# Optimization experiments

Hardware: AMD Instinct MI355X
Metric: run time of the kernel (lower is better)

The kernel has to match this reference:

```python
import jax, jax.numpy as jnp
import numpy as np

H = 256          # encoder hidden per direction
D = 2 * H        # decoder hidden / bidirectional feature dim
IN = 2
OUT = 2
B = 64
T = 256
STEPS = 24       # hard-coded decoder loop length in the source


def gru_cell(x, h, Wih, Whh, bih, bhh):
    # PyTorch GRU cell: gate order (r, z, n)
    gi = x @ Wih.T + bih
    gh = h @ Whh.T + bhh
    ir, iz, inn = jnp.split(gi, 3, axis=-1)
    hr, hz, hn = jnp.split(gh, 3, axis=-1)
    r = jax.nn.sigmoid(ir + hr)
    z = jax.nn.sigmoid(iz + hz)
    n = jnp.tanh(inn + r * hn)
    return (1.0 - z) * n + z * h


def run_dir(xs, Wih, Whh, bih, bhh, reverse):
    # xs: (T, B, F) time-major; returns outputs (T, B, H) and last hidden (B, H)
    h0 = jnp.zeros((xs.shape[1], Whh.shape[-1]), xs.dtype)
    def step(h, xt):
        h2 = gru_cell(xt, h, Wih, Whh, bih, bhh)
        return h2, h2
    h_last, ys = jax.lax.scan(step, h0, xs, reverse=reverse)
    return ys, h_last


def setup_inputs():
    keys = jax.random.split(jax.random.key(0), 24)
    k = iter(keys)
    def rn(shape, s):
        return jax.random.normal(next(k), shape, jnp.float32) * s
    se = 1.0 / np.sqrt(H)
    sd = 1.0 / np.sqrt(D)
    return {
        "x": rn((B, T, IN), 1.0),
        "enc_Wih0": rn((2, 3 * H, IN), se),
        "enc_Whh0": rn((2, 3 * H, H), se),
        "enc_bih0": rn((2, 3 * H), se),
        "enc_bhh0": rn((2, 3 * H), se),
        "enc_Wih": rn((2, 2, 3 * H, D), se),
        "enc_Whh": rn((2, 2, 3 * H, H), se),
        "enc_bih": rn((2, 2, 3 * H), se),
        "enc_bhh": rn((2, 2, 3 * H), se),
        "dec_Wih": rn((3, 3 * D, D), sd),
        "dec_Whh": rn((3, 3 * D, D), sd),
        "dec_bih": rn((3, 3 * D), sd),
        "dec_bhh": rn((3, 3 * D), sd),
        "fc_con_W": rn((D, 2 * D), sd),
        "fc_con_b": rn((D,), sd),
        "attn_W": rn((D, 2 * D), sd),
        "attn_b": rn((D,), sd),
        "v": jax.random.uniform(next(k), (D,), jnp.float32),  # torch.rand init
        "fc_W": rn((OUT, D), sd),
        "fc_b": rn((OUT,), sd),
    }


def reference(x, enc_Wih0, enc_Whh0, enc_bih0, enc_bhh0,
              enc_Wih, enc_Whh, enc_bih, enc_bhh,
              dec_Wih, dec_Whh, dec_bih, dec_bhh,
              fc_con_W, fc_con_b, attn_W, attn_b, v, fc_W, fc_b):
    # ---- bidirectional 3-layer GRU encoder ----
    seq = x.transpose(1, 0, 2)  # (T, B, IN) time-major
    hf_list, hb_list = [], []
    for l in range(3):
        if l == 0:
            Wf, Uf, bf, cf = enc_Wih0[0], enc_Whh0[0], enc_bih0[0], enc_bhh0[0]
            Wb, Ub, bb, cb = enc_Wih0[1], enc_Whh0[1], enc_bih0[1], enc_bhh0[1]
        else:
            Wf, Uf, bf, cf = enc_Wih[l-1, 0], enc_Whh[l-1, 0], enc_bih[l-1, 0], enc_bhh[l-1, 0]
            Wb, Ub, bb, cb = enc_Wih[l-1, 1], enc_Whh[l-1, 1], enc_bih[l-1, 1], enc_bhh[l-1, 1]
        yf, hf = run_dir(seq, Wf, Uf, bf, cf, False)
        yb, hb = run_dir(seq, Wb, Ub, bb, cb, True)
        seq = jnp.concatenate([yf, yb], axis=-1)
        hf_list.append(hf)
        hb_list.append(hb)
    enc_out = seq.transpose(1, 0, 2)  # (B, T, D)
    # hidden_decoder = cat(forward, backward) per layer -> (3, B, D)
    hidden = jnp.stack([jnp.concatenate([f, b], axis=-1)
                        for f, b in zip(hf_list, hb_list)])
    dec_in = enc_out[:, -1, :]  # (B, D)

    # additive attention: energy = tanh(W [h; enc_out] + b); precompute enc part
    attn_Wh = attn_W[:, :D]
    attn_We = attn_W[:, D:]
    enc_proj = jnp.einsum('bte,de->btd', enc_out, attn_We)  # (B, T, D)

    def dec_step(carry, _):
        d_in, hid = carry
        hq = hid[-1] @ attn_Wh.T                               # (B, D)
        energy = jnp.tanh(hq[:, None, :] + enc_proj + attn_b)  # (B, T, D)
        scores = jnp.einsum('btd,d->bt', energy, v)
        aw = jax.nn.softmax(scores, axis=1)                    # (B, T)
        ctx = jnp.einsum('bt,btd->bd', aw, enc_out)            # (B, D)
        inp = jnp.concatenate([d_in, ctx], axis=-1) @ fc_con_W.T + fc_con_b
        new_h = []
        for l in range(3):  # 3-layer unidirectional decoder GRU, single step
            hl = gru_cell(inp, hid[l], dec_Wih[l], dec_Whh[l], dec_bih[l], dec_bhh[l])
            new_h.append(hl)
            inp = hl
        out_step = inp @ fc_W.T + fc_b
        return (inp, jnp.stack(new_h)), out_step

    _, outs = jax.lax.scan(dec_step, (dec_in, hidden), None, length=STEPS)
    return outs.transpose(1, 0, 2)  # (B, 24, OUT)
```

## Files before the change

kernel.cpp:

```cpp
#include <hip/hip_runtime.h>

typedef unsigned short u16;
typedef unsigned int u32;
typedef _Float16 f16;
typedef f16   f16x2 __attribute__((ext_vector_type(2)));
typedef f16   f16x4 __attribute__((ext_vector_type(4)));
typedef f16   f16x8 __attribute__((ext_vector_type(8)));
typedef float f32x4 __attribute__((ext_vector_type(4)));

#define MFMA16(a,b,c) __builtin_amdgcn_mfma_f32_16x16x32_f16((a),(b),(c),0,0,0)

__device__ __forceinline__ float sigm_(float x){ return 1.f/(1.f + __expf(-x)); }
__device__ __forceinline__ float tanh_(float x){ return 1.f - 2.f/(1.f + __expf(2.f*x)); }
__device__ __forceinline__ float clampf(float x, float c){
  if (!(x > -c)) x = -c;
  if (x > c) x = c;
  return x;
}
__device__ __forceinline__ f16x8 cvt8f(const float* p){
  const float4 a = *(const float4*)p;
  const float4 b = *(const float4*)(p+4);
  f16x8 r;
  r[0]=(f16)a.x; r[1]=(f16)a.y; r[2]=(f16)a.z; r[3]=(f16)a.w;
  r[4]=(f16)b.x; r[5]=(f16)b.y; r[6]=(f16)b.z; r[7]=(f16)b.w;
  return r;
}

__device__ __forceinline__ void gbar_(u32* c, u32 nb){
  __syncthreads();
  __threadfence();
  if (threadIdx.x == 0) {
    __hip_atomic_fetch_add(c, 1u, __ATOMIC_RELAXED, __HIP_MEMORY_SCOPE_AGENT);
    while (__hip_atomic_load(c, __ATOMIC_RELAXED, __HIP_MEMORY_SCOPE_AGENT) < nb) {}
  }
  __syncthreads();
  __threadfence();
}

__global__ void k_diag(float* out, int mib){
  const int i = blockIdx.x*256 + threadIdx.x;
  if (i < 3072) out[i] = 1000.f * (float)mib;
}

__global__ void k_prep_dec(const float* dWhh, const float* attnW, const float* fccon,
                           const float* dWih, f16* R3)
{
  long idx = (long)blockIdx.x*256 + threadIdx.x;
  const float* src; int rs, colOff = 0, NKS; long dst, loc;
  if (idx < 294912L) {
    loc = idx; const int m = (int)(loc / 98304); loc %= 98304;
    src = dWhh + (long)m*786432; rs = 512; NKS = 16; dst = (long)m*786432;
  } else if (idx < 327680L) {
    loc = idx - 294912L; src = attnW; colOff = 512; rs = 1024; NKS = 16; dst = 2359296L;
  } else if (idx < 393216L) {
    loc = idx - 327680L; src = fccon; rs = 1024; NKS = 32; dst = 2621440L;
  } else if (idx < 688128L) {
    loc = idx - 393216L; const int m = (int)(loc / 98304); loc %= 98304;
    src = dWih + (long)m*786432; rs = 512; NKS = 16; dst = 3440640L + (long)m*786432;
  } else if (idx < 720896L) {
    loc = idx - 688128L; src = attnW; colOff = 0; rs = 1024; NKS = 16; dst = 5799936L;
  } else return;
  const int lane = (int)(loc & 63);
  const long frag = loc >> 6;
  const int ks = (int)(frag % NKS);
  const long nt = frag / NKS;
  const int n  = (int)(nt*16 + (lane & 15));
  const int k0 = ks*32 + ((lane >> 4) << 3);
  const float* sp = src + (long)n*rs + colOff + k0;
  f16* dp = R3 + dst + loc*8;
  #pragma unroll
  for (int j = 0; j < 8; ++j) dp[j] = (f16)sp[j];
}

__global__ void k_gi0s(const float* __restrict__ x, const float* __restrict__ W,
                       const float* __restrict__ bi, f16* __restrict__ gi,
                       int seg, int BH, int lbh, int b0)
{
  const long idx = (long)blockIdx.x*256 + threadIdx.x;
  const int v = (int)(idx % 24);
  long rest = idx / 24;
  const int tid = (int)(rest & 511); rest >>= 9;
  const int bq = (int)(rest & ((1 << (lbh-4)) - 1)); rest >>= (lbh-4);
  const int s = (int)(rest & 63);
  const int d = (int)(rest >> 6);
  const int r = v / 6, rem = v % 6, i = rem / 3, g = rem % 3;
  const int w = tid >> 6, q = (tid >> 4) & 3, lo = tid & 15;
  const int n = g*256 + (2*w + i)*16 + lo;
  const int b = bq*16 + q*4 + r;
  const int t = d ? (255 - (seg*64 + s)) : (seg*64 + s);
  const float x0 = x[(((b0+b)<<8) + t)*2];
  const float x1 = x[(((b0+b)<<8) + t)*2 + 1];
  const long wi = ((long)d*768 + n)*2;
  gi[idx] = (f16)clampf(x0*W[wi] + x1*W[wi+1] + bi[d*768 + n], 32.f);
}

#define GIE(G, vv) ((float)((vv) < 8 ? (G)[0][(vv)&7] : ((vv) < 16 ? (G)[1][(vv)-8] : (G)[2][(vv)-16])))

__global__ __launch_bounds__(512, 1) void k_enc_seg(
    const f16* __restrict__ gi, const float* __restrict__ Wraw,
    const float* __restrict__ bhh, f16* __restrict__ seq, int ostr,
    f16* __restrict__ fin, float* __restrict__ hcar, int seg, int BH)
{
  const int tid = threadIdx.x;
  const int w = tid >> 6, lane = tid & 63;
  const int lo16 = lane & 15, quad = lane >> 4;
  const int nbq = BH >> 4;
  const int dir = blockIdx.x / nbq, bq = blockIdx.x % nbq;

  __shared__ f16 h16[4][16][264];

  const float* mat = Wraw + (long)dir*196608;
  f16x8 wr[6][8];
  #pragma unroll
  for (int p = 0; p < 3; ++p)
    #pragma unroll
    for (int i = 0; i < 2; ++i) {
      const int n = (p*16 + 2*w + i)*16 + lo16;
      #pragma unroll
      for (int ks = 0; ks < 8; ++ks)
        wr[p*2+i][ks] = cvt8f(mat + (long)n*256 + ks*32 + quad*8);
    }
  float bh_[3][2];
  #pragma unroll
  for (int p = 0; p < 3; ++p)
    #pragma unroll
    for (int i = 0; i < 2; ++i)
      bh_[p][i] = bhh[dir*768 + p*256 + (2*w+i)*16 + lo16];

  float hreg[2][4];
  if (seg == 0) {
    #pragma unroll
    for (int i = 0; i < 2; ++i)
      #pragma unroll
      for (int r = 0; r < 4; ++r) {
        hreg[i][r] = 0.f;
        h16[0][quad*4 + r][(2*w+i)*16 + lo16] = (f16)0.f;
      }
  } else {
    #pragma unroll
    for (int i = 0; i < 2; ++i) {
      const int c = (2*w+i)*16 + lo16;
      #pragma unroll
      for (int r = 0; r < 4; ++r) {
        const float v = hcar[((dir*BH) + bq*16 + quad*4 + r)*256 + c];
        hreg[i][r] = v;
        h16[0][quad*4 + r][c] = (f16)v;
      }
    }
  }

  const long gstep = (long)nbq*512*24;
  const f16* gbase = gi + (((long)dir*64*nbq + bq)*512 + tid)*24;
  f16x8 g0[3], g1[3];
  { const f16x8* gp = (const f16x8*)gbase; g0[0]=gp[0]; g0[1]=gp[1]; g0[2]=gp[2]; }

  const int frow = tid >> 5;
  const int fcol = (tid & 31) * 8;

  for (int s = 0; s < 64; ++s) {
    __syncthreads();
    if (s >= 2) {
      const int so = s - 2;
      const int t2 = dir ? (255 - (seg*64 + so)) : (seg*64 + so);
      const f16x8 hv = *(const f16x8*)&h16[(so+1)&3][frow][fcol];
      *(f16x8*)&seq[((long)t2*ostr + bq*16 + frow)*512 + dir*256 + fcol] = hv;
    }
    f32x4 acc[6];
    #pragma unroll
    for (int q = 0; q < 6; ++q) acc[q] = (f32x4){0.f,0.f,0.f,0.f};
    #pragma unroll
    for (int ks = 0; ks < 8; ++ks) {
      const f16x8 a = *(const f16x8*)&h16[s&3][lo16][ks*32 + quad*8];
      #pragma unroll
      for (int q = 0; q < 6; ++q)
        acc[q] = MFMA16(a, wr[q][ks], acc[q]);
    }
    if (s < 63) {
      const f16x8* gp = (const f16x8*)(gbase + (long)(s+1)*gstep);
      g1[0]=gp[0]; g1[1]=gp[1]; g1[2]=gp[2];
    }
    #pragma unroll
    for (int i = 0; i < 2; ++i) {
      const int c = (2*w+i)*16 + lo16;
      #pragma unroll
      for (int r = 0; r < 4; ++r) {
        const int row = quad*4 + r;
        const int v = r*6 + i*3;
        const float gir = GIE(g0, v);
        const float giz = GIE(g0, v+1);
        const float gin = GIE(g0, v+2);
        const float rv = sigm_(gir + acc[i][r]   + bh_[0][i]);
        const float zv = sigm_(giz + acc[2+i][r] + bh_[1][i]);
        const float nv = tanh_(gin + rv*(acc[4+i][r] + bh_[2][i]));
        float hn = (1.f - zv)*nv + zv*hreg[i][r];
        hn = clampf(hn, 2.f);
        hreg[i][r] = hn;
        h16[(s+1)&3][row][c] = (f16)hn;
        if (seg == 3 && s == 63) fin[(bq*16 + row)*512 + dir*256 + c] = (f16)hn;
      }
    }
    g0[0]=g1[0]; g0[1]=g1[1]; g0[2]=g1[2];
  }
  __syncthreads();
  #pragma unroll
  for (int so = 62; so < 64; ++so) {
    const int t2 = dir ? (255 - (seg*64 + so)) : (seg*64 + so);
    const f16x8 hv = *(const f16x8*)&h16[(so+1)&3][frow][fcol];
    *(f16x8*)&seq[((long)t2*ostr + bq*16 + frow)*512 + dir*256 + fcol] = hv;
  }
  #pragma unroll
  for (int i = 0; i < 2; ++i) {
    const int c = (2*w+i)*16 + lo16;
    #pragma unroll
    for (int r = 0; r < 4; ++r)
      hcar[((dir*BH) + bq*16 + quad*4 + r)*256 + c] = hreg[i][r];
  }
}

__global__ void k_gemm_gi(const f16* __restrict__ A,
                          const float* __restrict__ Braw, long bzs,
                          const float* __restrict__ bias,
                          f16* __restrict__ gi,
                          int tb0, int tb1, int tdirsgn, int abstr, float cv)
{
  const int tid = threadIdx.x, w = tid>>6, lane = tid&63;
  const int lo16 = lane&15, quad = lane>>4;
  const int s_ = blockIdx.x;
  const int y  = blockIdx.y;
  const int z  = blockIdx.z;
  const int tbase = z ? tb1 : tb0;
  const int tdir  = z ? -tdirsgn : tdirsgn;
  const int mrow = s_*64 + w*16 + lo16;
  const long arow = (long)(tbase + tdir*(mrow >> 6))*abstr + (mrow & 63);
  const f16* Ap = A + arow*512 + quad*8;
  const float* Bp = Braw + (long)z*bzs;
  f32x4 acc[12];
  #pragma unroll
  for (int i=0;i<12;++i) acc[i]=(f32x4){0.f,0.f,0.f,0.f};
  for (int ks = 0; ks < 16; ++ks) {
    const f16x8 a = *(const f16x8*)(Ap + ks*32);
    #pragma unroll
    for (int g = 0; g < 3; ++g)
      #pragma unroll
      for (int jj = 0; jj < 4; ++jj) {
        const int n = g*256 + y*64 + jj*16 + lo16;
        const f16x8 b = cvt8f(Bp + (long)n*512 + ks*32 + quad*8);
        acc[g*4+jj] = MFMA16(a, b, acc[g*4+jj]);
      }
  }
  f16* base = gi + (((long)z*64 + s_)*4 + w)*12288L;
  #pragma unroll
  for (int l = 0; l < 2; ++l) {
    f16x8 rec8[3];
    #pragma unroll
    for (int r = 0; r < 4; ++r)
      #pragma unroll
      for (int jl = 0; jl < 2; ++jl)
        #pragma unroll
        for (int g = 0; g < 3; ++g) {
          const int nt = g*4 + l*2 + jl;
          const int n = g*256 + y*64 + (l*2+jl)*16 + lo16;
          const int slot = r*6 + jl*3 + g;
          rec8[slot>>3][slot&7] = (f16)clampf(acc[nt][r] + bias[z*768 + n], cv);
        }
    f16* dp = base + ((long)(y*2 + l)*64 + quad*16 + lo16)*24L;
    *(f16x8*)(dp)      = rec8[0];
    *(f16x8*)(dp + 8)  = rec8[1];
    *(f16x8*)(dp + 16) = rec8[2];
  }
}

__global__ void k_gemm(const f16* __restrict__ A, int K,
                       const f16* __restrict__ Bsw, const float* __restrict__ Braw,
                       long bzs, int ldb, int koff,
                       const float* __restrict__ bias, int biaszs,
                       void* __restrict__ Cv, long czs, int ldc, int mode,
                       int tb0, int tb1, int tdirsgn, int lbh, int abstr, float cv)
{
  const int tid = threadIdx.x, w = tid>>6, lane = tid&63;
  const int lo16 = lane&15, quad = lane>>4;
  const int m0 = blockIdx.x*64 + w*16;
  const int n0 = blockIdx.y*128;
  const int z  = blockIdx.z;
  const int tbase = z ? tb1 : tb0;
  const int tdir  = z ? -tdirsgn : tdirsgn;
  const int NKS = K >> 5;
  const int mrow = m0 + lo16;
  const long arow = (long)(tbase + tdir*(mrow >> lbh))*abstr + (mrow & ((1<<lbh)-1));
  const f16* Ap = A + arow*K + quad*8;
  f32x4 acc[8];
  #pragma unroll
  for (int i=0;i<8;++i) acc[i]=(f32x4){0.f,0.f,0.f,0.f};
  if (Bsw) {
    const f16* Bp = Bsw + (long)z*bzs;
    for (int ks = 0; ks < NKS; ++ks) {
      const f16x8 a = *(const f16x8*)(Ap + ks*32);
      #pragma unroll
      for (int nt = 0; nt < 8; ++nt) {
        const f16x8 b = *(const f16x8*)(Bp + (((long)((n0>>4)+nt)*NKS + ks) << 9) + lane*8);
        acc[nt] = MFMA16(a, b, acc[nt]);
      }
    }
  } else {
    const float* Bp = Braw + (long)z*bzs;
    for (int ks = 0; ks < NKS; ++ks) {
      const f16x8 a = *(const f16x8*)(Ap + ks*32);
      #pragma unroll
      for (int nt = 0; nt < 8; ++nt) {
        const f16x8 b = cvt8f(Bp + (long)(n0 + nt*16 + lo16)*ldb + koff + ks*32 + quad*8);
        acc[nt] = MFMA16(a, b, acc[nt]);
      }
    }
  }
  #pragma unroll
  for (int nt = 0; nt < 8; ++nt) {
    const int n = n0 + nt*16 + lo16;
    const float bv = bias ? bias[z*biaszs + n] : 0.f;
    #pragma unroll
    for (int r = 0; r < 4; ++r) {
      const int m = m0 + quad*4 + r;
      const float val = clampf(acc[nt][r] + bv, cv);
      if (mode == 2) {
        const int s_ = m >> lbh, b_ = m & ((1<<lbh)-1);
        const int bq_ = b_ >> 4, q_ = (b_ >> 2) & 3, r_ = b_ & 3;
        const int g_ = n >> 8, j_ = (n >> 4) & 15, lo_ = n & 15;
        const long idx = ((((long)z*64 + s_)*(1<<(lbh-4)) + bq_)*512
                          + ((j_>>1)*64 + q_*16 + lo_))*24 + r_*6 + (j_&1)*3 + g_;
        ((f16*)Cv)[idx] = (f16)val;
      } else if (mode == 1)
        ((f16*)Cv)[(long)z*czs + (long)m*ldc + n] = (f16)val;
      else
        ((float*)Cv)[(long)z*czs + (long)m*ldc + n] = val;
    }
  }
}

__global__ void k_score(const f16* __restrict__ seq, const f16* __restrict__ We,
                        const float* __restrict__ hq, const float* __restrict__ ab,
                        const float* __restrict__ vp, float* __restrict__ S)
{
  const int t = blockIdx.x, tid = threadIdx.x;
  const int w = tid>>6, lane = tid&63, lo16 = lane&15, quad = lane>>4;
  __shared__ float svab[1024];
  for (int i = tid; i < 512; i += 256) { svab[i] = vp[i]; svab[512+i] = ab[i]; }
  __syncthreads();
  f32x4 acc[32];
  #pragma unroll
  for (int i=0;i<32;++i) acc[i]=(f32x4){0.f,0.f,0.f,0.f};
  const f16* Ap = seq + ((long)t*64 + w*16 + lo16)*512 + quad*8;
  for (int ks = 0; ks < 16; ++ks) {
    const f16x8 a = *(const f16x8*)(Ap + ks*32);
    #pragma unroll
    for (int nt = 0; nt < 32; ++nt) {
      const f16x8 b = *(const f16x8*)(We + (((long)nt*16 + ks) << 9) + lane*8);
      acc[nt] = MFMA16(a, b, acc[nt]);
    }
  }
  #pragma unroll
  for (int r = 0; r < 4; ++r) {
    const int b = w*16 + quad*4 + r;
    float sc = 0.f;
    #pragma unroll
    for (int nt = 0; nt < 32; ++nt) {
      const int n = nt*16 + lo16;
      sc += svab[n] * tanh_(acc[nt][r] + hq[(b<<9) + n] + svab[512+n]);
    }
    sc += __shfl_xor(sc, 1, 64); sc += __shfl_xor(sc, 2, 64);
    sc += __shfl_xor(sc, 4, 64); sc += __shfl_xor(sc, 8, 64);
    if (lo16 == 0) S[(b<<8) + t] = clampf(sc, 256.f);
  }
}

__global__ void k_attnctx(const float* __restrict__ S, const f16* __restrict__ enc,
                          f16* __restrict__ cat)
{
  const int b = blockIdx.x, tid = threadIdx.x;
  __shared__ float ssc[256], srd[256];
  const float sc = clampf(S[(b<<8) + tid], 256.f);
  srd[tid] = sc; __syncthreads();
  for (int off = 128; off > 0; off >>= 1) { if (tid < off) srd[tid] = fmaxf(srd[tid], srd[tid+off]); __syncthreads(); }
  const float mx = srd[0]; __syncthreads();
  const float e = __expf(sc - mx);
  srd[tid] = e; __syncthreads();
  for (int off = 128; off > 0; off >>= 1) { if (tid < off) srd[tid] += srd[tid+off]; __syncthreads(); }
  const float inv = 1.f / srd[0]; __syncthreads();
  ssc[tid] = e * inv; __syncthreads();
  float c0 = 0.f, c1 = 0.f;
  for (int tt = 0; tt < 256; ++tt) {
    const float awt = ssc[tt];
    const f16* ep = enc + (((long)tt*64 + b) << 9);
    c0 += awt * (float)ep[tid];
    c1 += awt * (float)ep[256 + tid];
  }
  cat[(b<<10) + 512 + tid] = (f16)clampf(c0, 4.f);
  cat[(b<<10) + 768 + tid] = (f16)clampf(c1, 4.f);
}

__global__ void k_dec_init(const f16* __restrict__ fin, const f16* __restrict__ seq,
                           f16* __restrict__ hb16, float* __restrict__ hf32,
                           f16* __restrict__ cat, u32* __restrict__ cnt)
{
  const int idx = blockIdx.x*256 + threadIdx.x;
  if (idx < 64) cnt[idx] = 0;
  const int d = idx & 511, b = (idx >> 9) & 63, l = idx >> 15;
  if (l < 3) {
    const float v = clampf((float)fin[((long)l<<15) + (b<<9) + d], 2.f);
    hb16[(long)l*65536 + (b<<9) + d] = (f16)v;
    hf32[(long)l*32768 + (b<<9) + d] = v;
  } else {
    cat[(b<<10) + d] = seq[((long)255*64 + b)*512 + d];
  }
}

__global__ __launch_bounds__(512, 1) void k_attn(
    const f16* __restrict__ seq, const f16* __restrict__ ep,
    const float* __restrict__ hf2, const f16* __restrict__ cat,
    const f16* __restrict__ whsw, const f16* __restrict__ fcsw,
    const float* __restrict__ fcconB, const float* __restrict__ vp,
    f16* __restrict__ inp, const float* __restrict__ fcW,
    const float* __restrict__ fcb, float* __restrict__ out, int step)
{
  const int b = blockIdx.x;
  const int tid = threadIdx.x, w = tid >> 6, lane = tid & 63;
  const int quad = lane >> 4;
  __shared__ float hsm[512];
  __shared__ float cats[1024];
  __shared__ float hqs[512];
  __shared__ float aw[256];
  __shared__ float red[8*512];
  hsm[tid]  = hf2[(b<<9) + tid];
  cats[tid] = (float)cat[(b<<10) + tid];
  __syncthreads();
  if (w < 2 && step > 0) {
    float p = 0.f;
    #pragma unroll
    for (int j = 0; j < 8; ++j) p += fcW[(w<<9) + lane*8 + j] * hsm[lane*8 + j];
    p += __shfl_xor(p,1,64); p += __shfl_xor(p,2,64); p += __shfl_xor(p,4,64);
    p += __shfl_xor(p,8,64); p += __shfl_xor(p,16,64); p += __shfl_xor(p,32,64);
    if (lane == 0) out[(b*24 + step-1)*2 + w] = clampf(p + fcb[w], 128.f);
  }
  #pragma unroll
  for (int i = 0; i < 4; ++i) {
    const int nt = w*4 + i;
    float p = 0.f;
    for (int ks = 0; ks < 16; ++ks) {
      const f16x8 wv = *(const f16x8*)(whsw + (((long)nt*16 + ks)<<9) + lane*8);
      const float4 ha = *(const float4*)&hsm[ks*32 + quad*8];
      const float4 hb = *(const float4*)&hsm[ks*32 + quad*8 + 4];
      p += (float)wv[0]*ha.x + (float)wv[1]*ha.y + (float)wv[2]*ha.z + (float)wv[3]*ha.w
         + (float)wv[4]*hb.x + (float)wv[5]*hb.y + (float)wv[6]*hb.z + (float)wv[7]*hb.w;
    }
    p += __shfl_xor(p,16,64); p += __shfl_xor(p,32,64);
    if (lane < 16) hqs[nt*16 + lane] = p;
  }
  __syncthreads();
  float hq8[8], v8[8];
  #pragma unroll
  for (int j = 0; j < 8; ++j) { hq8[j] = hqs[lane*8+j]; v8[j] = vp[lane*8+j]; }
  #pragma unroll 2
  for (int i = 0; i < 32; ++i) {
    const int t = w*32 + i;
    const f16x8 e = *(const f16x8*)(ep + (((long)t*64 + b)<<9) + lane*8);
    float s = 0.f;
    #pragma unroll
    for (int j = 0; j < 8; ++j) s += v8[j]*tanh_((float)e[j] + hq8[j]);
    s += __shfl_xor(s,1,64); s += __shfl_xor(s,2,64); s += __shfl_xor(s,4,64);
    s += __shfl_xor(s,8,64); s += __shfl_xor(s,16,64); s += __shfl_xor(s,32,64);
    if (lane == 0) aw[t] = clampf(s, 256.f);
  }
  __syncthreads();
  if (tid < 64) {
    float s0=aw[tid], s1=aw[tid+64], s2=aw[tid+128], s3=aw[tid+192];
    float mx = fmaxf(fmaxf(s0,s1), fmaxf(s2,s3));
    mx = fmaxf(mx, __shfl_xor(mx,1,64)); mx = fmaxf(mx, __shfl_xor(mx,2,64));
    mx = fmaxf(mx, __shfl_xor(mx,4,64)); mx = fmaxf(mx, __shfl_xor(mx,8,64));
    mx = fmaxf(mx, __shfl_xor(mx,16,64)); mx = fmaxf(mx, __shfl_xor(mx,32,64));
    const float e0=__expf(s0-mx), e1=__expf(s1-mx), e2=__expf(s2-mx), e3=__expf(s3-mx);
    float sm = e0+e1+e2+e3;
    sm += __shfl_xor(sm,1,64); sm += __shfl_xor(sm,2,64); sm += __shfl_xor(sm,4,64);
    sm += __shfl_xor(sm,8,64); sm += __shfl_xor(sm,16,64); sm += __shfl_xor(sm,32,64);
    const float inv = 1.f/sm;
    aw[tid]=e0*inv; aw[tid+64]=e1*inv; aw[tid+128]=e2*inv; aw[tid+192]=e3*inv;
  }
  __syncthreads();
  float c8[8];
  #pragma unroll
  for (int j = 0; j < 8; ++j) c8[j] = 0.f;
  #pragma unroll 2
  for (int i = 0; i < 32; ++i) {
    const int t = w*32 + i;
    const f16x8 e = *(const f16x8*)(seq + (((long)t*64 + b)<<9) + lane*8);
    const float awt = aw[t];
    #pragma unroll
    for (int j = 0; j < 8; ++j) c8[j] += awt*(float)e[j];
  }
  #pragma unroll
  for (int j = 0; j < 8; ++j) red[(w<<9) + lane*8 + j] = c8[j];
  __syncthreads();
  {
    float s = 0.f;
    #pragma unroll
    for (int ww = 0; ww < 8; ++ww) s += red[(ww<<9) + tid];
    cats[512 + tid] = clampf(s, 4.f);
  }
  __syncthreads();
  #pragma unroll
  for (int i = 0; i < 4; ++i) {
    const int nt = w*4 + i;
    float p = 0.f;
    for (int ks = 0; ks < 32; ++ks) {
      const f16x8 wv = *(const f16x8*)(fcsw + (((long)nt*32 + ks)<<9) + lane*8);
      const float4 ca = *(const float4*)&cats[ks*32 + quad*8];
      const float4 cb = *(const float4*)&cats[ks*32 + quad*8 + 4];
      p += (float)wv[0]*ca.x + (float)wv[1]*ca.y + (float)wv[2]*ca.z + (float)wv[3]*ca.w
         + (float)wv[4]*cb.x + (float)wv[5]*cb.y + (float)wv[6]*cb.z + (float)wv[7]*cb.w;
    }
    p += __shfl_xor(p,16,64); p += __shfl_xor(p,32,64);
    if (lane < 16) inp[(b<<9) + nt*16 + lane] = (f16)clampf(p + fcconB[nt*16+lane], 64.f);
  }
}

__global__ void k_cell3(const f16* __restrict__ inp0, const f16* __restrict__ WihSw,
                        const f16* __restrict__ WhhSw, const float* __restrict__ bihA,
                        const float* __restrict__ bhhA, float* __restrict__ hfA,
                        f16* __restrict__ hb, f16* __restrict__ cat, int p, u32* cnt)
{
  const int tid = threadIdx.x, w = tid>>6, lane = tid&63;
  const int lo16 = lane&15, quad = lane>>4;
  const int Wt  = ((int)blockIdx.x & 7)*4 + w;
  const int mi0 = ((int)blockIdx.x >> 3)*2;
  for (int l = 0; l < 3; ++l) {
    const f16* inp = (l == 0) ? inp0 : (hb + (long)(2*(l-1) + (1-p))*32768);
    const f16* WihL = WihSw + (long)l*786432;
    const f16* WhhL = WhhSw + (long)l*786432;
    const float* bih = bihA + l*1536;
    const float* bhh = bhhA + l*1536;
    float* hf32 = hfA + (long)l*32768;
    const f16* hin = hb + (long)(2*l + p)*32768;
    f16* hout = hb + (long)(2*l + (1-p))*32768;
    f16* catp = (l == 2) ? cat : (f16*)nullptr;

    f32x4 arz[4], an_[4];
    #pragma unroll
    for (int i=0;i<4;++i){ arz[i]=(f32x4){0.f,0.f,0.f,0.f}; an_[i]=(f32x4){0.f,0.f,0.f,0.f}; }
    #pragma unroll 2
    for (int kk = 0; kk < 16; ++kk) {
      const f16x8 b0 = *(const f16x8*)(WihL + (((long)Wt*16 + kk)<<9)      + lane*8);
      const f16x8 b1 = *(const f16x8*)(WihL + (((long)(32+Wt)*16 + kk)<<9) + lane*8);
      const f16x8 b2 = *(const f16x8*)(WihL + (((long)(64+Wt)*16 + kk)<<9) + lane*8);
      #pragma unroll
      for (int m = 0; m < 2; ++m) {
        const f16x8 a = *(const f16x8*)&inp[(((mi0+m)*16 + lo16)<<9) + kk*32 + quad*8];
        arz[m]   = MFMA16(a, b0, arz[m]);
        arz[2+m] = MFMA16(a, b1, arz[2+m]);
        an_[m]   = MFMA16(a, b2, an_[m]);
      }
    }
    #pragma unroll 2
    for (int kk = 0; kk < 16; ++kk) {
      const f16x8 b0 = *(const f16x8*)(WhhL + (((long)Wt*16 + kk)<<9)      + lane*8);
      const f16x8 b1 = *(const f16x8*)(WhhL + (((long)(32+Wt)*16 + kk)<<9) + lane*8);
      const f16x8 b2 = *(const f16x8*)(WhhL + (((long)(64+Wt)*16 + kk)<<9) + lane*8);
      #pragma unroll
      for (int m = 0; m < 2; ++m) {
        const f16x8 a = *(const f16x8*)&hin[(((mi0+m)*16 + lo16)<<9) + kk*32 + quad*8];
        arz[m]   = MFMA16(a, b0, arz[m]);
        arz[2+m] = MFMA16(a, b1, arz[2+m]);
        an_[2+m] = MFMA16(a, b2, an_[2+m]);
      }
    }
    const int c = Wt*16 + lo16;
    const float brz0 = bih[c]     + bhh[c];
    const float brz1 = bih[512+c] + bhh[512+c];
    const float bin_ = bih[1024+c];
    const float bhn_ = bhh[1024+c];
    #pragma unroll
    for (int m = 0; m < 2; ++m)
      #pragma unroll
      for (int r = 0; r < 4; ++r) {
        const int row = (mi0+m)*16 + quad*4 + r;
        const float rv = sigm_(clampf(arz[m][r],64.f)   + brz0);
        const float zv = sigm_(clampf(arz[2+m][r],64.f) + brz1);
        const float nv = tanh_(clampf(an_[m][r],64.f) + bin_ + rv*(clampf(an_[2+m][r],64.f) + bhn_));
        const float ho = hf32[(row<<9) + c];
        float hn2 = (1.f - zv)*nv + zv*ho;
        hn2 = clampf(hn2, 2.f);
        hf32[(row<<9) + c] = hn2;
        hout[(row<<9) + c] = (f16)hn2;
        if (catp) catp[(row<<10) + c] = (f16)hn2;
      }
    if (l < 2) gbar_(cnt + l, 16);
  }
}

__global__ void k_cell_raw(const f16* __restrict__ inp, const float* __restrict__ WihRaw,
                           const f16* __restrict__ WhhSw, const float* __restrict__ bih,
                           const float* __restrict__ bhh, float* __restrict__ hf32,
                           const f16* __restrict__ hin, f16* __restrict__ hout,
                           f16* __restrict__ cat)
{
  const int tid = threadIdx.x, w = tid>>6, lane = tid&63;
  const int lo16 = lane&15, quad = lane>>4;
  const int Wt = blockIdx.x*4 + w;
  f32x4 arz[8], an_[8];
  #pragma unroll
  for (int i=0;i<8;++i){ arz[i]=(f32x4){0.f,0.f,0.f,0.f}; an_[i]=(f32x4){0.f,0.f,0.f,0.f}; }
  const int nr = Wt*16 + lo16;
  const float* Rr = WihRaw + (long)nr*512        + quad*8;
  const float* Rz = WihRaw + (long)(512+nr)*512  + quad*8;
  const float* Rn = WihRaw + (long)(1024+nr)*512 + quad*8;
  #pragma unroll 2
  for (int kk = 0; kk < 16; ++kk) {
    const f16x8 b0 = cvt8f(Rr + kk*32);
    const f16x8 b1 = cvt8f(Rz + kk*32);
    const f16x8 b2 = cvt8f(Rn + kk*32);
    #pragma unroll
    for (int mi = 0; mi < 4; ++mi) {
      const f16x8 a = *(const f16x8*)&inp[((mi*16 + lo16)<<9) + kk*32 + quad*8];
      arz[mi]   = MFMA16(a, b0, arz[mi]);
      arz[4+mi] = MFMA16(a, b1, arz[4+mi]);
      an_[mi]   = MFMA16(a, b2, an_[mi]);
    }
  }
  #pragma unroll 2
  for (int kk = 0; kk < 16; ++kk) {
    const f16x8 b0 = *(const f16x8*)(WhhSw + (((long)Wt*16 + kk)<<9)      + lane*8);
    const f16x8 b1 = *(const f16x8*)(WhhSw + (((long)(32+Wt)*16 + kk)<<9) + lane*8);
    const f16x8 b2 = *(const f16x8*)(WhhSw + (((long)(64+Wt)*16 + kk)<<9) + lane*8);
    #pragma unroll
    for (int mi = 0; mi < 4; ++mi) {
      const f16x8 a = *(const f16x8*)&hin[((mi*16 + lo16)<<9) + kk*32 + quad*8];
      arz[mi]   = MFMA16(a, b0, arz[mi]);
      arz[4+mi] = MFMA16(a, b1, arz[4+mi]);
      an_[4+mi] = MFMA16(a, b2, an_[4+mi]);
    }
  }
  const int c = Wt*16 + lo16;
  const float brz0 = bih[c]     + bhh[c];
  const float brz1 = bih[512+c] + bhh[512+c];
  const float bin_ = bih[1024+c];
  const float bhn_ = bhh[1024+c];
  #pragma unroll
  for (int mi = 0; mi < 4; ++mi)
    #pragma unroll
    for (int r = 0; r < 4; ++r) {
      const int row = mi*16 + quad*4 + r;
      const float rv = sigm_(clampf(arz[mi][r],64.f)   + brz0);
      const float zv = sigm_(clampf(arz[4+mi][r],64.f) + brz1);
      const float nv = tanh_(clampf(an_[mi][r],64.f) + bin_ + rv*(clampf(an_[4+mi][r],64.f) + bhn_));
      const float ho = hf32[(row<<9) + c];
      float hn2 = (1.f - zv)*nv + zv*ho;
      hn2 = clampf(hn2, 2.f);
      hf32[(row<<9) + c] = hn2;
      hout[(row<<9) + c] = (f16)hn2;
      if (cat) cat[(row<<10) + c] = (f16)hn2;
    }
}

__global__ void k_out(const float* __restrict__ h2, const float* __restrict__ fcW,
                      const float* __restrict__ fcb, float* __restrict__ out, int step)
{
  const int b = blockIdx.x, t = threadIdx.x;
  __shared__ float r0[256], r1[256];
  const float ha = clampf(h2[(b<<9) + t], 2.f);
  const float hb = clampf(h2[(b<<9) + 256 + t], 2.f);
  r0[t] = ha*fcW[t]     + hb*fcW[256+t];
  r1[t] = ha*fcW[512+t] + hb*fcW[768+t];
  __syncthreads();
  for (int off = 128; off > 0; off >>= 1) {
    if (t < off) { r0[t] += r0[t+off]; r1[t] += r1[t+off]; }
    __syncthreads();
  }
  if (t == 0) {
    out[(b*24 + step)*2]     = clampf(r0[0] + fcb[0], 128.f);
    out[(b*24 + step)*2 + 1] = clampf(r1[0] + fcb[1], 128.f);
  }
}

extern "C" void kernel_launch(void* const* d_in, const int* in_sizes, int n_in,
                              void* d_out, int out_size, void* d_ws, size_t ws_size,
                              hipStream_t stream) {
  const float* X      = (const float*)d_in[0];
  const float* eWih0  = (const float*)d_in[1];
  const float* eWhh0  = (const float*)d_in[2];
  const float* ebih0  = (const float*)d_in[3];
  const float* ebhh0  = (const float*)d_in[4];
  const float* eWih   = (const float*)d_in[5];
  const float* eWhh   = (const float*)d_in[6];
  const float* ebih   = (const float*)d_in[7];
  const float* ebhh   = (const float*)d_in[8];
  const float* dWih   = (const float*)d_in[9];
  const float* dWhh   = (const float*)d_in[10];
  const float* dbih   = (const float*)d_in[11];
  const float* dbhh   = (const float*)d_in[12];
  const float* fcconW = (const float*)d_in[13];
  const float* fcconB = (const float*)d_in[14];
  const float* attnW  = (const float*)d_in[15];
  const float* attnB  = (const float*)d_in[16];
  const float* vW     = (const float*)d_in[17];
  const float* fcW    = (const float*)d_in[18];
  const float* fcB    = (const float*)d_in[19];
  float* OUT = (float*)d_out;

  const long need_big  = 47054848L;
  const long need_half = 32964608L;
  f16* H = (f16*)d_ws;
  f16 *SEQ = H, *L1OUT, *GIB, *R3, *FIN, *HB, *CAT, *INP;
  float *HC;
  int BH, lbh, nh, l1ostr, l1abstr; long gdir;

  if ((long)ws_size >= need_big) {
    BH = 64; lbh = 6; nh = 1; l1ostr = 64; l1abstr = 64;
    L1OUT = H + 8388608L;
    GIB   = H + 16777216L;
    HC    = (float*)(H + 23068672L);
    FIN   = H + 23134208L;
    HB    = H + 23232512L;
    CAT   = H + 23429120L;
    INP   = H + 23494656L;
    gdir  = 3145728L;
  } else if ((long)ws_size >= need_half) {
    BH = 32; lbh = 5; nh = 2; l1ostr = 32; l1abstr = 32;
    L1OUT = H + 8388608L;
    GIB   = H + 12582912L;
    HC    = (float*)(H + 16023552L);
    FIN   = H + 16089088L;
    HB    = H + 16187392L;
    CAT   = H + 16384000L;
    INP   = H + 16449536L;
    gdir  = 1572864L;
  } else {
    k_diag<<<12, 256, 0, stream>>>(OUT, (int)(ws_size >> 20));
    return;
  }
  R3 = GIB;
  float* ST = (float*)(GIB + 3145728L);
  float* HQ = ST;
  float* HF = ST + 32768;
  float* S  = ST + 131072;
  u32* CNT = (u32*)ST;
  const int nblk = 2*(BH>>4);
  const int gi0grid = (2*64*BH*768)/256;

  for (int h = 0; h < nh; ++h) {
    const int b0 = h*BH;
    for (int seg = 0; seg < 4; ++seg) {
      k_gi0s<<<gi0grid, 256, 0, stream>>>(X, eWih0, ebih0, GIB, seg, BH, lbh, b0);
      k_enc_seg<<<nblk, 512, 0, stream>>>(GIB, eWhh0, ebhh0, SEQ + (long)b0*512, 64,
                                          FIN + (long)b0*512, HC, seg, BH);
    }
    for (int seg = 0; seg < 4; ++seg) {
      if (BH == 64)
        k_gemm_gi<<<dim3(64, 4, 2), 256, 0, stream>>>(SEQ, eWih, 393216L, ebih,
            GIB, seg*64, 255 - seg*64, 1, 64, 32.f);
      else
        k_gemm<<<dim3(BH, 6, 2), 256, 0, stream>>>(SEQ + (long)b0*512, 512,
            (const f16*)nullptr, eWih, 393216L, 512, 0, ebih, 768,
            GIB, gdir, 768, 2, seg*64, 255 - seg*64, 1, lbh, 64, 32.f);
      k_enc_seg<<<nblk, 512, 0, stream>>>(GIB, eWhh, ebhh, L1OUT, l1ostr,
                                          FIN + 32768 + (long)b0*512, HC, seg, BH);
    }
    for (int seg = 0; seg < 4; ++seg) {
      if (BH == 64)
        k_gemm_gi<<<dim3(64, 4, 2), 256, 0, stream>>>(L1OUT, eWih + 2L*393216,
            393216L, ebih + 1536, GIB, seg*64, 255 - seg*64, 1, 64, 32.f);
      else
        k_gemm<<<dim3(BH, 6, 2), 256, 0, stream>>>(L1OUT, 512,
            (const f16*)nullptr, eWih + 2L*393216, 393216L, 512, 0, ebih + 1536, 768,
            GIB, gdir, 768, 2, seg*64, 255 - seg*64, 1, lbh, l1abstr, 32.f);
      k_enc_seg<<<nblk, 512, 0, stream>>>(GIB, eWhh + 2L*196608, ebhh + 1536,
                                          SEQ + (long)b0*512, 64,
                                          FIN + 65536 + (long)b0*512, HC, seg, BH);
    }
  }

  if (BH == 64) {
    f16* EP    = L1OUT;
    f16* WIHSW = GIB + 3440640L;
    f16* WHSW  = GIB + 5799936L;

    k_prep_dec<<<2816, 256, 0, stream>>>(dWhh, attnW, fcconW, dWih, R3);
    k_gemm<<<dim3(256, 4, 1), 256, 0, stream>>>(SEQ, 512,
        R3 + 2359296L, (const float*)nullptr, 0L, 0, 0, attnB, 0,
        EP, 0L, 512, 1, 0, 0, 1, 6, 64, 32.f);
    k_dec_init<<<512, 256, 0, stream>>>(FIN, SEQ, HB, HF, CAT, CNT);

    for (int s = 0; s < 24; ++s) {
      const int p = s & 1;
      k_attn<<<64, 512, 0, stream>>>(SEQ, EP, HF + 2*32768, CAT, WHSW, R3 + 2621440L,
          fcconB, vW, INP, fcW, fcB, OUT, s);
      k_cell3<<<16, 256, 0, stream>>>(INP, WIHSW, R3, dbih, dbhh, HF, HB, CAT,
          p, CNT + s*2);
    }
    k_out<<<64, 256, 0, stream>>>(HF + 2*32768, fcW, fcB, OUT, 23);
  } else {
    k_prep_dec<<<1536, 256, 0, stream>>>(dWhh, attnW, fcconW, dWih, R3);
    k_dec_init<<<512, 256, 0, stream>>>(FIN, SEQ, HB, HF, CAT, (u32*)(S + 16000));

    for (int s = 0; s < 24; ++s) {
      const int p = s & 1;
      const f16* h2in = HB + (4 + p)*32768L;
      k_gemm<<<dim3(1,4,1), 256, 0, stream>>>(h2in, 512,
          (const f16*)nullptr, attnW, 0L, 1024, 0, (const float*)nullptr, 0,
          HQ, 0L, 512, 0, 0, 0, 0, 6, 64, 64.f);
      k_score<<<256, 256, 0, stream>>>(SEQ, R3 + 2359296L, HQ, attnB, vW, S);
      k_attnctx<<<64, 256, 0, stream>>>(S, SEQ, CAT);
      k_gemm<<<dim3(1,4,1), 256, 0, stream>>>(CAT, 1024,
          R3 + 2621440L, (const float*)nullptr, 0L, 0, 0, fcconB, 0,
          INP, 0L, 512, 1, 0, 0, 0, 6, 64, 64.f);
      for (int l = 0; l < 3; ++l) {
        const f16* inp = (l == 0) ? INP : (HB + (2*(l-1) + (1-p))*32768L);
        k_cell_raw<<<8, 256, 0, stream>>>(inp,
                  dWih + (long)l*786432, R3 + (long)l*786432,
                  dbih + l*1536, dbhh + l*1536, HF + (long)l*32768,
                  HB + (2*l + p)*32768L, HB + (2*l + (1-p))*32768L,
                  (l == 2) ? CAT : (f16*)nullptr);
      }
      k_out<<<64, 256, 0, stream>>>(HF + 2*32768, fcW, fcB, OUT, s);
    }
  }
}
```

Measured before the change: 6.218 ms.

## Split decoder GRU cell over more blocks and store attention projection batch-major

The decoder cell kernel now launches 32 blocks, each handling one 16-row batch tile instead of two, so twice as many CUs share the weight streaming and each wave keeps fewer accumulators. The grid barrier count changes to match. Separately, the encoder attention projection GEMM gains an output mode that writes the result batch-major, (b, t) rather than (t, b). The score loop in the attention kernel then reads each batch's timesteps contiguously. The trade-off is that every weight tile is now loaded by twice as many blocks, and the grid barrier must synchronise more participants.

After: 6.068 ms. 1.02x faster.

```diff
diff --git a/kernel.cpp b/kernel.cpp
--- a/kernel.cpp
+++ b/kernel.cpp
@@ -327,7 +327,9 @@
         const long idx = ((((long)z*64 + s_)*(1<<(lbh-4)) + bq_)*512
                           + ((j_>>1)*64 + q_*16 + lo_))*24 + r_*6 + (j_&1)*3 + g_;
         ((f16*)Cv)[idx] = (f16)val;
-      } else if (mode == 1)
+      } else if (mode == 3)
+        ((f16*)Cv)[(((long)(m & 63) << 8) + (m >> 6))*512 + n] = (f16)val;
+      else if (mode == 1)
         ((f16*)Cv)[(long)z*czs + (long)m*ldc + n] = (f16)val;
       else
         ((float*)Cv)[(long)z*czs + (long)m*ldc + n] = val;
@@ -460,7 +462,7 @@
   #pragma unroll 2
   for (int i = 0; i < 32; ++i) {
     const int t = w*32 + i;
-    const f16x8 e = *(const f16x8*)(ep + (((long)t*64 + b)<<9) + lane*8);
+    const f16x8 e = *(const f16x8*)(ep + (((long)(b<<8) + t)<<9) + lane*8);
     float s = 0.f;
     #pragma unroll
     for (int j = 0; j < 8; ++j) s += v8[j]*tanh_((float)e[j] + hq8[j]);
@@ -527,8 +529,8 @@
 {
   const int tid = threadIdx.x, w = tid>>6, lane = tid&63;
   const int lo16 = lane&15, quad = lane>>4;
-  const int Wt  = ((int)blockIdx.x & 7)*4 + w;
-  const int mi0 = ((int)blockIdx.x >> 3)*2;
+  const int Wt = ((int)blockIdx.x & 7)*4 + w;
+  const int mi = (int)blockIdx.x >> 3;
   for (int l = 0; l < 3; ++l) {
     const f16* inp = (l == 0) ? inp0 : (hb + (long)(2*(l-1) + (1-p))*32768);
     const f16* WihL = WihSw + (long)l*786432;
@@ -540,34 +542,28 @@
     f16* hout = hb + (long)(2*l + (1-p))*32768;
     f16* catp = (l == 2) ? cat : (f16*)nullptr;
 
-    f32x4 arz[4], an_[4];
-    #pragma unroll
-    for (int i=0;i<4;++i){ arz[i]=(f32x4){0.f,0.f,0.f,0.f}; an_[i]=(f32x4){0.f,0.f,0.f,0.f}; }
-    #pragma unroll 2
+    f32x4 arz[2], an_[2];
+    #pragma unroll
+    for (int i=0;i<2;++i){ arz[i]=(f32x4){0.f,0.f,0.f,0.f}; an_[i]=(f32x4){0.f,0.f,0.f,0.f}; }
+    #pragma unroll 4
     for (int kk = 0; kk < 16; ++kk) {
       const f16x8 b0 = *(const f16x8*)(WihL + (((long)Wt*16 + kk)<<9)      + lane*8);
       const f16x8 b1 = *(const f16x8*)(WihL + (((long)(32+Wt)*16 + kk)<<9) + lane*8);
       const f16x8 b2 = *(const f16x8*)(WihL + (((long)(64+Wt)*16 + kk)<<9) + lane*8);
-      #pragma unroll
-      for (int m = 0; m < 2; ++m) {
-        const f16x8 a = *(const f16x8*)&inp[(((mi0+m)*16 + lo16)<<9) + kk*32 + quad*8];
-        arz[m]   = MFMA16(a, b0, arz[m]);
-        arz[2+m] = MFMA16(a, b1, arz[2+m]);
-        an_[m]   = MFMA16(a, b2, an_[m]);
-      }
-    }
-    #pragma unroll 2
+      const f16x8 a = *(const f16x8*)&inp[((mi*16 + lo16)<<9) + kk*32 + quad*8];
+      arz[0] = MFMA16(a, b0, arz[0]);
+      arz[1] = MFMA16(a, b1, arz[1]);
+      an_[0] = MFMA16(a, b2, an_[0]);
+    }
+    #pragma unroll 4
     for (int kk = 0; kk < 16; ++kk) {
       const f16x8 b0 = *(const f16x8*)(WhhL + (((long)Wt*16 + kk)<<9)      + lane*8);
       const f16x8 b1 = *(const f16x8*)(WhhL + (((long)(32+Wt)*16 + kk)<<9) + lane*8);
       const f16x8 b2 = *(const f16x8*)(WhhL + (((long)(64+Wt)*16 + kk)<<9) + lane*8);
-      #pragma unroll
-      for (int m = 0; m < 2; ++m) {
-        const f16x8 a = *(const f16x8*)&hin[(((mi0+m)*16 + lo16)<<9) + kk*32 + quad*8];
-        arz[m]   = MFMA16(a, b0, arz[m]);
-        arz[2+m] = MFMA16(a, b1, arz[2+m]);
-        an_[2+m] = MFMA16(a, b2, an_[2+m]);
-      }
+      const f16x8 a = *(const f16x8*)&hin[((mi*16 + lo16)<<9) + kk*32 + quad*8];
+      arz[0] = MFMA16(a, b0, arz[0]);
+      arz[1] = MFMA16(a, b1, arz[1]);
+      an_[1] = MFMA16(a, b2, an_[1]);
     }
     const int c = Wt*16 + lo16;
     const float brz0 = bih[c]     + bhh[c];
@@ -575,21 +571,19 @@
     const float bin_ = bih[1024+c];
     const float bhn_ = bhh[1024+c];
     #pragma unroll
-    for (int m = 0; m < 2; ++m)
-      #pragma unroll
-      for (int r = 0; r < 4; ++r) {
-        const int row = (mi0+m)*16 + quad*4 + r;
-        const float rv = sigm_(clampf(arz[m][r],64.f)   + brz0);
-        const float zv = sigm_(clampf(arz[2+m][r],64.f) + brz1);
-        const float nv = tanh_(clampf(an_[m][r],64.f) + bin_ + rv*(clampf(an_[2+m][r],64.f) + bhn_));
-        const float ho = hf32[(row<<9) + c];
-        float hn2 = (1.f - zv)*nv + zv*ho;
-        hn2 = clampf(hn2, 2.f);
-        hf32[(row<<9) + c] = hn2;
-        hout[(row<<9) + c] = (f16)hn2;
-        if (catp) catp[(row<<10) + c] = (f16)hn2;
-      }
-    if (l < 2) gbar_(cnt + l, 16);
+    for (int r = 0; r < 4; ++r) {
+      const int row = mi*16 + quad*4 + r;
+      const float rv = sigm_(clampf(arz[0][r],64.f) + brz0);
+      const float zv = sigm_(clampf(arz[1][r],64.f) + brz1);
+      const float nv = tanh_(clampf(an_[0][r],64.f) + bin_ + rv*(clampf(an_[1][r],64.f) + bhn_));
+      const float ho = hf32[(row<<9) + c];
+      float hn2 = (1.f - zv)*nv + zv*ho;
+      hn2 = clampf(hn2, 2.f);
+      hf32[(row<<9) + c] = hn2;
+      hout[(row<<9) + c] = (f16)hn2;
+      if (catp) catp[(row<<10) + c] = (f16)hn2;
+    }
+    if (l < 2) gbar_(cnt + l, 32);
   }
 }
 
@@ -782,14 +776,14 @@
     k_prep_dec<<<2816, 256, 0, stream>>>(dWhh, attnW, fcconW, dWih, R3);
     k_gemm<<<dim3(256, 4, 1), 256, 0, stream>>>(SEQ, 512,
         R3 + 2359296L, (const float*)nullptr, 0L, 0, 0, attnB, 0,
-        EP, 0L, 512, 1, 0, 0, 1, 6, 64, 32.f);
+        EP, 0L, 512, 3, 0, 0, 1, 6, 64, 32.f);
     k_dec_init<<<512, 256, 0, stream>>>(FIN, SEQ, HB, HF, CAT, CNT);
 
     for (int s = 0; s < 24; ++s) {
       const int p = s & 1;
       k_attn<<<64, 512, 0, stream>>>(SEQ, EP, HF + 2*32768, CAT, WHSW, R3 + 2621440L,
           fcconB, vW, INP, fcW, fcB, OUT, s);
-      k_cell3<<<16, 256, 0, stream>>>(INP, WIHSW, R3, dbih, dbhh, HF, HB, CAT,
+      k_cell3<<<32, 256, 0, stream>>>(INP, WIHSW, R3, dbih, dbhh, HF, HB, CAT,
           p, CNT + s*2);
     }
     k_out<<<64, 256, 0, stream>>>(HF + 2*32768, fcW, fcB, OUT, 23);
```
